# Performance work log

Measured on AMD Instinct MI355X. Metric: run time of the kernel, lower is better.

Reference implementation:

```python
import jax, jax.numpy as jnp
import numpy as np

B, C, H, W = 8, 64, 64, 64
HID = 256  # hidden width of gate_strength_fc


def _init_params(key):
    ks = jax.random.split(key, 12)
    s = 0.05
    p = {}
    p['Wq'] = jax.random.normal(ks[0], (C, C), jnp.float32) * s
    p['bq'] = jnp.zeros((C,), jnp.float32)
    p['Wk'] = jax.random.normal(ks[1], (C, C), jnp.float32) * s
    p['bk'] = jnp.zeros((C,), jnp.float32)
    p['Wv'] = jax.random.normal(ks[2], (C, C), jnp.float32) * s
    p['bv'] = jnp.zeros((C,), jnp.float32)
    p['Wg'] = jax.random.normal(ks[3], (C, C), jnp.float32) * s
    p['bg'] = jnp.zeros((C,), jnp.float32)
    p['W1'] = jax.random.normal(ks[4], (HID, C), jnp.float32) * s
    p['b1'] = jnp.zeros((HID,), jnp.float32)
    p['W2'] = jax.random.normal(ks[5], (1, HID), jnp.float32) * s
    p['b2'] = jnp.zeros((1,), jnp.float32)
    return p


def setup_inputs() -> dict:
    key = jax.random.key(0)
    k0, k1, k2, kp = jax.random.split(key, 4)
    x = jax.random.normal(k0, (B, C, H, W), jnp.float32)
    # torch.rand(...) > 0.8 dropout-style mask, precomputed as 0/1 float for determinism
    mask = (jax.random.uniform(k1, (B, 1, H, W), jnp.float32) > 0.8).astype(jnp.float32)
    use_entropy_gate = jax.random.bernoulli(k2, 0.5, (B,))
    inp = {'x': x, 'mask': mask, 'use_entropy_gate': use_entropy_gate}
    inp.update(_init_params(kp))
    return inp


def _conv1x1(w, b, t):
    # 1x1 conv == per-pixel matmul over channels
    return jnp.einsum('oc,bchw->bohw', w, t) + b[None, :, None, None]


def reference(x, mask, use_entropy_gate, Wq, bq, Wk, bk, Wv, bv, Wg, bg, W1, b1, W2, b2):
    b_, c_, h_, w_ = x.shape
    n = h_ * w_
    masked_x = x * mask
    q = _conv1x1(Wq, bq, masked_x).reshape(b_, c_, n).transpose(0, 2, 1)  # [B,N,C]
    k = _conv1x1(Wk, bk, masked_x).reshape(b_, c_, n)                      # [B,C,N]
    v = _conv1x1(Wv, bv, x).reshape(b_, c_, n)                             # [B,C,N]
    attn = jax.nn.softmax(jnp.einsum('bnc,bcm->bnm', q, k), axis=-1)       # [B,N,N]
    out = jnp.einsum('bcn,bmn->bcm', v, attn).reshape(b_, c_, h_, w_)
    hidden = jax.nn.relu(_conv1x1(W1, b1, x))
    gate_strength = jax.nn.sigmoid(_conv1x1(W2, b2, hidden))               # [B,1,H,W]
    gate = jax.nn.sigmoid(_conv1x1(Wg, bg, x))                             # [B,C,H,W]
    flag = use_entropy_gate[:, None, None, None]
    return jnp.where(flag, out * gate * gate_strength, x)
```

## Files before the change

### kernel.cpp

```cpp
#include <hip/hip_runtime.h>
#include <hip/hip_bf16.h>
#include <math.h>

namespace {
constexpr int kB = 8;
constexpr int kC = 64;
constexpr int kN = 4096;
constexpr int kCap = 1280;
constexpr int kQS = 1312;
constexpr int kSplit = 4;
constexpr long kSeg = (long)kB * kC * kN;
typedef __attribute__((ext_vector_type(8))) short short8;
typedef __attribute__((ext_vector_type(4))) float f32x4;
}

__global__ __launch_bounds__(256) void prep_compact_kernel(
    const float* __restrict__ mask,
    const float* __restrict__ Wq, const float* __restrict__ Wk,
    const float* __restrict__ Wv, const float* __restrict__ Wg,
    const float* __restrict__ W1,
    const float* __restrict__ bq, const float* __restrict__ bk,
    const float* __restrict__ bv, const float* __restrict__ bg,
    const float* __restrict__ b1,
    int* __restrict__ p2i, int* __restrict__ cnt,
    __hip_bfloat16* __restrict__ Wfrag, float* __restrict__ bias_all) {
  const int t = threadIdx.x;
  if (blockIdx.x < kB) {
    const int b = blockIdx.x;
    __shared__ int sc_[256];
    const int base = b * kN + t * 16;
    unsigned flags = 0;
    int c16 = 0;
#pragma unroll
    for (int u = 0; u < 16; ++u) {
      const int a = (mask[base + u] != 0.f) ? 1 : 0;
      flags |= (unsigned)a << u;
      c16 += a;
    }
    sc_[t] = c16;
    __syncthreads();
    for (int off = 1; off < 256; off <<= 1) {
      const int v = (t >= off) ? sc_[t - off] : 0;
      __syncthreads();
      sc_[t] += v;
      __syncthreads();
    }
    int rank = sc_[t] - c16;
#pragma unroll
    for (int u = 0; u < 16; ++u) {
      const int n = t * 16 + u;
      const int a = (flags >> u) & 1;
      int r = -1;
      if (a) {
        if (rank < kCap) r = rank;
        rank += 1;
      }
      p2i[b * kN + n] = r;
    }
    if (t == 255) cnt[b] = sc_[255];
    return;
  }
  const int e = (blockIdx.x - kB) * 256 + t;
  const int mt = e >> 7;
  const int ks = (e >> 6) & 1;
  const int lane = e & 63;
  const int m = mt * 16 + (lane & 15);
  const int k0 = ks * 32 + (lane >> 4) * 8;
  const float* Wsrc;
  int row;
  if (m < 64)       { Wsrc = Wq; row = m; }
  else if (m < 128) { Wsrc = Wk; row = m - 64; }
  else if (m < 192) { Wsrc = Wv; row = m - 128; }
  else if (m < 256) { Wsrc = Wg; row = m - 192; }
  else              { Wsrc = W1; row = m - 256; }
#pragma unroll
  for (int j = 0; j < 8; ++j)
    Wfrag[(long)e * 8 + j] = __float2bfloat16(Wsrc[row * kC + k0 + j]);
  if (e < 512) {
    float bb;
    if (e < 64)       bb = bq[e];
    else if (e < 128) bb = bk[e - 64];
    else if (e < 192) bb = bv[e - 128];
    else if (e < 256) bb = bg[e - 192];
    else              bb = b1[e - 256];
    bias_all[e] = bb;
  }
}

__global__ __launch_bounds__(256) void dense_kernel(
    const float* __restrict__ x, const float* __restrict__ mask,
    const int* __restrict__ flag, const int* __restrict__ p2i,
    const __hip_bfloat16* __restrict__ Wfrag, const float* __restrict__ bias_all,
    const float* __restrict__ W2, const float* __restrict__ b2,
    __hip_bfloat16* __restrict__ G, float* __restrict__ GS,
    __hip_bfloat16* __restrict__ Qa, __hip_bfloat16* __restrict__ Ka,
    __hip_bfloat16* __restrict__ VaT, float* __restrict__ Sq,
    float* __restrict__ xmsP) {
  const int b = blockIdx.y;
  if (!flag[b]) return;
  const int n0 = blockIdx.x * 64;
  const int t = threadIdx.x;

  __shared__ __hip_bfloat16 sX[64][72];
  __shared__ float sB[512];
  __shared__ float sW2[256];
  {
    const int c = t >> 2;
    const int nn = (t & 3) * 16;
    const float* xp = x + (long)b * kC * kN + (long)c * kN + n0 + nn;
#pragma unroll
    for (int u = 0; u < 16; ++u) sX[nn + u][c] = __float2bfloat16(xp[u]);
  }
  sB[t] = bias_all[t];
  sB[t + 256] = bias_all[t + 256];
  sW2[t] = W2[t];
  __syncthreads();

  const int w = t >> 6;
  const int lane = t & 63;
  const int col = lane & 15;
  const int quad = lane >> 4;
  const int nl = w * 16 + col;
  const int n = n0 + nl;

  const short8 bfr0 = *(const short8*)&sX[nl][quad * 8];
  const short8 bfr1 = *(const short8*)&sX[nl][32 + quad * 8];

  const int i_act = p2i[b * kN + n];
  const float b2v = b2[0];

  float gs_acc = 0.f;
  float sq_acc = 0.f;
  for (int mt = 0; mt < 32; ++mt) {
    f32x4 acc = {0.f, 0.f, 0.f, 0.f};
    const short8 a0 = *(const short8*)(Wfrag + (((long)(mt * 2 + 0) * 64 + lane) * 8));
    const short8 a1 = *(const short8*)(Wfrag + (((long)(mt * 2 + 1) * 64 + lane) * 8));
    acc = __builtin_amdgcn_mfma_f32_16x16x32_bf16(a0, bfr0, acc, 0, 0, 0);
    acc = __builtin_amdgcn_mfma_f32_16x16x32_bf16(a1, bfr1, acc, 0, 0, 0);
    const int rbase = mt * 16 + quad * 4;
    if (mt < 4) {
      if (i_act >= 0) {
#pragma unroll
        for (int g = 0; g < 4; ++g) {
          const int r = rbase + g;
          const float qv = acc[g] + sB[r];
          Qa[((long)b * kCap + i_act) * kC + r] = __float2bfloat16(qv);
          sq_acc += qv * sB[64 + r];
        }
      }
    } else if (mt < 8) {
      if (i_act >= 0) {
#pragma unroll
        for (int g = 0; g < 4; ++g) {
          const int r = rbase + g;
          Ka[((long)b * kCap + i_act) * kC + (r - 64)] = __float2bfloat16(acc[g] + sB[r]);
        }
      }
    } else if (mt < 12) {
      if (i_act >= 0) {
#pragma unroll
        for (int g = 0; g < 4; ++g) {
          const int r = rbase + g;
          VaT[((long)b * kC + (r - 128)) * kCap + i_act] =
              __float2bfloat16(acc[g] + sB[r]);
        }
      }
    } else if (mt < 16) {
#pragma unroll
      for (int g = 0; g < 4; ++g) {
        const int r = rbase + g;
        const float gv = 1.f / (1.f + __expf(-(acc[g] + sB[r])));
        G[((long)b * kC + (r - 192)) * kN + n] = __float2bfloat16(gv);
      }
    } else {
#pragma unroll
      for (int g = 0; g < 4; ++g) {
        const int r = rbase + g;
        gs_acc += sW2[r - 256] * fmaxf(acc[g] + sB[r], 0.f);
      }
    }
  }
  gs_acc += __shfl_xor(gs_acc, 16);
  gs_acc += __shfl_xor(gs_acc, 32);
  sq_acc += __shfl_xor(sq_acc, 16);
  sq_acc += __shfl_xor(sq_acc, 32);
  if (quad == 0) {
    GS[(long)b * kN + n] = 1.f / (1.f + __expf(-(gs_acc + b2v)));
    if (i_act >= 0) Sq[(long)b * kCap + i_act] = sq_acc;
  }

  {
    const int c = t >> 2;
    const int g4 = t & 3;
    const float* mp = mask + (long)b * kN + n0 + g4 * 16;
    float s = 0.f;
#pragma unroll
    for (int u = 0; u < 16; ++u)
      if (mp[u] == 0.f) s += __bfloat162float(sX[g4 * 16 + u][c]);
    s += __shfl_xor(s, 1);
    s += __shfl_xor(s, 2);
    if (g4 == 0) xmsP[((long)b * 64 + blockIdx.x) * kC + c] = s;
  }
}

__global__ __launch_bounds__(64) void attn_act_kernel(
    const __hip_bfloat16* __restrict__ Qa, const __hip_bfloat16* __restrict__ Ka,
    const __hip_bfloat16* __restrict__ VaT,
    const int* __restrict__ cnt, const int* __restrict__ flag,
    const float* __restrict__ bq, const float* __restrict__ bk,
    const float* __restrict__ bv, const float* __restrict__ Wv,
    const float* __restrict__ xmsP,
    float* __restrict__ Pm, float* __restrict__ Pl,
    __hip_bfloat16* __restrict__ Po,
    float* __restrict__ Vsum, float* __restrict__ s0M) {
  const int b = blockIdx.z;
  if (!flag[b]) return;
  const int lane = threadIdx.x;

  __shared__ __hip_bfloat16 sP[16][40];
  __shared__ float sxm[kC];

  if (blockIdx.x == kQS / 16) {
    if (blockIdx.y != 0) return;
    float acc = 0.f;
    for (int k = 0; k < 64; ++k) acc += xmsP[((long)b * 64 + k) * kC + lane];
    sxm[lane] = acc;
    __syncthreads();
    float v = 0.f;
#pragma unroll
    for (int o = 0; o < kC; ++o) v += Wv[lane * kC + o] * sxm[o];
    Vsum[b * kC + lane] = v + (float)(kN - cnt[b]) * bv[lane];
    float pp = bq[lane] * bk[lane];
#pragma unroll
    for (int d = 1; d < 64; d <<= 1) pp += __shfl_xor(pp, d);
    if (lane == 0) s0M[0] = pp;
    return;
  }

  const int cc = min(cnt[b], kCap);
  const int ccq = cc + 1;
  const int q0 = blockIdx.x * 16;
  if (q0 >= ccq) return;
  const int s = blockIdx.y;
  const int col = lane & 15;
  const int quad = lane >> 4;
  const int gq = q0 + col;

  const int nT = (cc + 31) >> 5;
  const int tq = (nT + kSplit - 1) / kSplit;
  const int t0 = s * tq;
  const int t1 = min(t0 + tq, nT);
  const long pb = ((long)b * kSplit + s) * kQS + gq;

  if (t0 >= t1) {
    if (gq < ccq) {
      if (quad == 0) { Pm[pb] = -3e38f; Pl[pb] = 0.f; }
#pragma unroll
      for (int ct = 0; ct < 4; ++ct)
#pragma unroll
        for (int g = 0; g < 4; ++g)
          Po[pb * kC + ct * 16 + quad * 4 + g] = __float2bfloat16(0.f);
    }
    return;
  }

  short8 qf0, qf1;
  if (gq == cc) {
#pragma unroll
    for (int j = 0; j < 8; ++j) {
      ((__hip_bfloat16*)&qf0)[j] = __float2bfloat16(bq[quad * 8 + j]);
      ((__hip_bfloat16*)&qf1)[j] = __float2bfloat16(bq[32 + quad * 8 + j]);
    }
  } else {
    const int qrow = (gq < cc) ? gq : (cc - 1);
    const __hip_bfloat16* qr = Qa + ((long)b * kCap + qrow) * kC + quad * 8;
    qf0 = *(const short8*)(qr);
    qf1 = *(const short8*)(qr + 32);
  }

  float Mi = -3e38f, Li = 0.f;
  f32x4 oacc[4];
#pragma unroll
  for (int ct = 0; ct < 4; ++ct) oacc[ct] = (f32x4){0.f, 0.f, 0.f, 0.f};

  for (int kt = t0; kt < t1; ++kt) {
    const int i0 = kt * 32;
    const int kr0 = min(i0 + col, cc - 1);
    const int kr1 = min(i0 + 16 + col, cc - 1);
    const __hip_bfloat16* kp0 = Ka + ((long)b * kCap + kr0) * kC + quad * 8;
    const __hip_bfloat16* kp1 = Ka + ((long)b * kCap + kr1) * kC + quad * 8;
    const short8 kf00 = *(const short8*)(kp0);
    const short8 kf01 = *(const short8*)(kp0 + 32);
    const short8 kf10 = *(const short8*)(kp1);
    const short8 kf11 = *(const short8*)(kp1 + 32);

    f32x4 sa0 = {0.f, 0.f, 0.f, 0.f}, sa1 = {0.f, 0.f, 0.f, 0.f};
    sa0 = __builtin_amdgcn_mfma_f32_16x16x32_bf16(kf00, qf0, sa0, 0, 0, 0);
    sa0 = __builtin_amdgcn_mfma_f32_16x16x32_bf16(kf01, qf1, sa0, 0, 0, 0);
    sa1 = __builtin_amdgcn_mfma_f32_16x16x32_bf16(kf10, qf0, sa1, 0, 0, 0);
    sa1 = __builtin_amdgcn_mfma_f32_16x16x32_bf16(kf11, qf1, sa1, 0, 0, 0);

    float sc[8];
#pragma unroll
    for (int g = 0; g < 4; ++g) {
      sc[g]     = (i0 + quad * 4 + g < cc)      ? sa0[g] : -3e38f;
      sc[4 + g] = (i0 + 16 + quad * 4 + g < cc) ? sa1[g] : -3e38f;
    }
    float lm = sc[0];
#pragma unroll
    for (int u = 1; u < 8; ++u) lm = fmaxf(lm, sc[u]);
    lm = fmaxf(lm, __shfl_xor(lm, 16));
    lm = fmaxf(lm, __shfl_xor(lm, 32));
    const float newM = fmaxf(Mi, lm);
    const float alpha = __expf(Mi - newM);
    float p[8], ps = 0.f;
#pragma unroll
    for (int u = 0; u < 8; ++u) { p[u] = __expf(sc[u] - newM); ps += p[u]; }
    ps += __shfl_xor(ps, 16);
    ps += __shfl_xor(ps, 32);
    Li = Li * alpha + ps;
    Mi = newM;

#pragma unroll
    for (int g = 0; g < 4; ++g) {
      sP[col][quad * 4 + g] = __float2bfloat16(p[g]);
      sP[col][16 + quad * 4 + g] = __float2bfloat16(p[4 + g]);
    }
    __syncthreads();
    const short8 pf = *(const short8*)&sP[col][quad * 8];

#pragma unroll
    for (int ct = 0; ct < 4; ++ct)
#pragma unroll
      for (int g = 0; g < 4; ++g) oacc[ct][g] *= alpha;
#pragma unroll
    for (int ct = 0; ct < 4; ++ct) {
      const short8 vf = *(const short8*)(
          VaT + ((long)b * kC + ct * 16 + col) * kCap + i0 + quad * 8);
      oacc[ct] = __builtin_amdgcn_mfma_f32_16x16x32_bf16(vf, pf, oacc[ct], 0, 0, 0);
    }
    __syncthreads();
  }

  if (gq < ccq) {
    if (quad == 0) { Pm[pb] = Mi; Pl[pb] = Li; }
#pragma unroll
    for (int ct = 0; ct < 4; ++ct)
#pragma unroll
      for (int g = 0; g < 4; ++g)
        Po[pb * kC + ct * 16 + quad * 4 + g] = __float2bfloat16(oacc[ct][g]);
  }
}

__global__ __launch_bounds__(256) void epilogue_kernel(
    const float* __restrict__ x, const int* __restrict__ flag,
    const int* __restrict__ p2i, const int* __restrict__ cnt,
    const float* __restrict__ Pm, const float* __restrict__ Pl,
    const __hip_bfloat16* __restrict__ Po, const float* __restrict__ Sq,
    const float* __restrict__ s0M, const float* __restrict__ Vsum,
    const __hip_bfloat16* __restrict__ G, const float* __restrict__ GS,
    float* __restrict__ out) {
  const int b = blockIdx.z;
  const int cg = blockIdx.y;
  const int n = blockIdx.x * 256 + threadIdx.x;
  const int t = threadIdx.x;
  const long bbase = (long)b * kC * kN + n;
  if (!flag[b]) {
#pragma unroll
    for (int u = 0; u < 16; ++u) {
      const long a = bbase + (long)(cg * 16 + u) * kN;
      out[a] = x[a];
    }
    return;
  }
  const int cTrue = cnt[b];
  const int cc = min(cTrue, kCap);
  const float multF = (float)(kN - cTrue);

  __shared__ float sFac[5];
  __shared__ float sOM16[16];
  __shared__ float sVs[16];
  if (t == 0) {
    const float s0 = s0M[0];
    float mar[kSplit], lar[kSplit];
    float M = s0;
#pragma unroll
    for (int s = 0; s < kSplit; ++s) {
      const long pbs = ((long)b * kSplit + s) * kQS + cc;
      mar[s] = Pm[pbs];
      lar[s] = Pl[pbs];
      M = fmaxf(M, mar[s]);
    }
    const float p0 = __expf(s0 - M);
    float L = multF * p0;
    float wgt[kSplit];
#pragma unroll
    for (int s = 0; s < kSplit; ++s) { wgt[s] = __expf(mar[s] - M); L += lar[s] * wgt[s]; }
    const float invL = 1.f / L;
#pragma unroll
    for (int s = 0; s < kSplit; ++s) sFac[s] = wgt[s] * invL;
    sFac[4] = p0 * invL;
  }
  if (t < 16) sVs[t] = Vsum[b * kC + cg * 16 + t];
  __syncthreads();
  if (t < 16) {
    const int c = cg * 16 + t;
    float o = sFac[4] * sVs[t];
#pragma unroll
    for (int s = 0; s < kSplit; ++s)
      o += sFac[s] * __bfloat162float(Po[(((long)b * kSplit + s) * kQS + cc) * kC + c]);
    sOM16[t] = o;
  }
  __syncthreads();

  const float gsv = GS[(long)b * kN + n];
  const int i = p2i[b * kN + n];
  float fac[kSplit], facP = 0.f;
  if (i >= 0) {
    const float s0 = Sq[(long)b * kCap + i];
    float mar[kSplit], lar[kSplit];
    float M = s0;
#pragma unroll
    for (int s = 0; s < kSplit; ++s) {
      const long pbs = ((long)b * kSplit + s) * kQS + i;
      mar[s] = Pm[pbs];
      lar[s] = Pl[pbs];
      M = fmaxf(M, mar[s]);
    }
    const float p0 = __expf(s0 - M);
    float L = multF * p0;
#pragma unroll
    for (int s = 0; s < kSplit; ++s) { fac[s] = __expf(mar[s] - M); L += lar[s] * fac[s]; }
    const float invL = 1.f / L;
#pragma unroll
    for (int s = 0; s < kSplit; ++s) fac[s] *= invL;
    facP = p0 * invL;
  }
#pragma unroll
  for (int u = 0; u < 16; ++u) {
    const int c = cg * 16 + u;
    float r;
    if (i >= 0) {
      r = facP * sVs[u];
#pragma unroll
      for (int s = 0; s < kSplit; ++s)
        r += fac[s] * __bfloat162float(Po[(((long)b * kSplit + s) * kQS + i) * kC + c]);
    } else {
      r = sOM16[u];
    }
    const long a = bbase + (long)c * kN;
    out[a] = r * __bfloat162float(G[a]) * gsv;
  }
}

extern "C" void kernel_launch(void* const* d_in, const int* in_sizes, int n_in,
                              void* d_out, int out_size, void* d_ws, size_t ws_size,
                              hipStream_t stream) {
  (void)in_sizes; (void)n_in; (void)out_size; (void)ws_size;
  const float* x    = (const float*)d_in[0];
  const float* mask = (const float*)d_in[1];
  const int*   flag = (const int*)d_in[2];
  const float* Wq = (const float*)d_in[3];
  const float* bq = (const float*)d_in[4];
  const float* Wk = (const float*)d_in[5];
  const float* bk = (const float*)d_in[6];
  const float* Wv = (const float*)d_in[7];
  const float* bv = (const float*)d_in[8];
  const float* Wg = (const float*)d_in[9];
  const float* bg = (const float*)d_in[10];
  const float* W1 = (const float*)d_in[11];
  const float* b1 = (const float*)d_in[12];
  const float* W2 = (const float*)d_in[13];
  const float* b2 = (const float*)d_in[14];
  float* out = (float*)d_out;

  char* w = (char*)d_ws;
  float* GS = (float*)w;                       w += (long)kB * kN * 4;
  __hip_bfloat16* G  = (__hip_bfloat16*)w;     w += kSeg * 2;
  __hip_bfloat16* Qa = (__hip_bfloat16*)w;     w += (long)kB * kCap * kC * 2;
  __hip_bfloat16* Ka = (__hip_bfloat16*)w;     w += (long)kB * kCap * kC * 2;
  __hip_bfloat16* VaT= (__hip_bfloat16*)w;     w += (long)kB * kC * kCap * 2;
  __hip_bfloat16* Po = (__hip_bfloat16*)w;     w += (long)kB * kSplit * kQS * kC * 2;
  float* Pm = (float*)w;                       w += (long)kB * kSplit * kQS * 4;
  float* Pl = (float*)w;                       w += (long)kB * kSplit * kQS * 4;
  float* Sq = (float*)w;                       w += (long)kB * kCap * 4;
  float* xmsP = (float*)w;                     w += (long)kB * 64 * kC * 4;
  __hip_bfloat16* Wfrag=(__hip_bfloat16*)w;    w += (long)512 * 64 * 2;
  float* bias_all = (float*)w;                 w += 512 * 4;
  int* p2i = (int*)w;                          w += (long)kB * kN * 4;
  int* cnt = (int*)w;                          w += 64;
  float* Vsum = (float*)w;                     w += kB * kC * 4;
  float* s0M  = (float*)w;                     w += 64;

  prep_compact_kernel<<<kB + 16, 256, 0, stream>>>(
      mask, Wq, Wk, Wv, Wg, W1, bq, bk, bv, bg, b1, p2i, cnt, Wfrag, bias_all);
  dim3 gd(kN / 64, kB);
  dense_kernel<<<gd, 256, 0, stream>>>(x, mask, flag, p2i, Wfrag, bias_all, W2, b2,
                                       G, GS, Qa, Ka, VaT, Sq, xmsP);
  dim3 gat(kQS / 16 + 1, kSplit, kB);
  attn_act_kernel<<<gat, 64, 0, stream>>>(Qa, Ka, VaT, cnt, flag, bq, bk, bv, Wv,
                                          xmsP, Pm, Pl, Po, Vsum, s0M);
  dim3 gep(kN / 256, 4, kB);
  epilogue_kernel<<<gep, 256, 0, stream>>>(x, flag, p2i, cnt, Pm, Pl, Po, Sq,
                                           s0M, Vsum, G, GS, out);
}
```

Baseline: 129.4 us.

## Fuse all stages into one cooperative persistent kernel with grid syncs

Replaces the four separate launches (prep/compact, dense projections, attention, epilogue) with a single cooperative kernel of 512 blocks that moves between phases using grid-wide syncs. Mask compaction is now done per tile with a prefix count plus ballot instead of a separate scan kernel. Weights are converted to bf16 fragments on the fly rather than prepacked. The attention phase uses per-wave shared buffers and no longer needs block barriers. The aim is to remove launch gaps and inter-kernel drain, at the cost of grid sync overhead, redundant prefix counting over the mask, and limited parallelism in the attention phase.

```diff
diff --git a/kernel.cpp b/kernel.cpp
--- a/kernel.cpp
+++ b/kernel.cpp
@@ -1,6 +1,9 @@
 #include <hip/hip_runtime.h>
+#include <hip/hip_cooperative_groups.h>
 #include <hip/hip_bf16.h>
 #include <math.h>
+
+namespace cg = cooperative_groups;
 
 namespace {
 constexpr int kB = 8;
@@ -9,447 +12,405 @@
 constexpr int kCap = 1280;
 constexpr int kQS = 1312;
 constexpr int kSplit = 4;
+constexpr int kQT = kQS / 16;
+constexpr int kAttnW = kQT * kSplit * kB;
+constexpr int kGrid = 512;
 constexpr long kSeg = (long)kB * kC * kN;
 typedef __attribute__((ext_vector_type(8))) short short8;
 typedef __attribute__((ext_vector_type(4))) float f32x4;
 }
 
-__global__ __launch_bounds__(256) void prep_compact_kernel(
-    const float* __restrict__ mask,
-    const float* __restrict__ Wq, const float* __restrict__ Wk,
-    const float* __restrict__ Wv, const float* __restrict__ Wg,
-    const float* __restrict__ W1,
-    const float* __restrict__ bq, const float* __restrict__ bk,
-    const float* __restrict__ bv, const float* __restrict__ bg,
-    const float* __restrict__ b1,
-    int* __restrict__ p2i, int* __restrict__ cnt,
-    __hip_bfloat16* __restrict__ Wfrag, float* __restrict__ bias_all) {
+__global__ __launch_bounds__(256, 2) void fused_kernel(
+    const float* __restrict__ x, const float* __restrict__ mask,
+    const int* __restrict__ flag,
+    const float* __restrict__ Wq, const float* __restrict__ bq,
+    const float* __restrict__ Wk, const float* __restrict__ bk,
+    const float* __restrict__ Wv, const float* __restrict__ bv,
+    const float* __restrict__ Wg, const float* __restrict__ bg,
+    const float* __restrict__ W1, const float* __restrict__ b1,
+    const float* __restrict__ W2, const float* __restrict__ b2,
+    float* __restrict__ out,
+    float* __restrict__ GS, __hip_bfloat16* __restrict__ G,
+    __hip_bfloat16* __restrict__ Qa, __hip_bfloat16* __restrict__ Ka,
+    __hip_bfloat16* __restrict__ VaT,
+    __hip_bfloat16* __restrict__ Po, float* __restrict__ Pm,
+    float* __restrict__ Pl, float* __restrict__ Sq,
+    float* __restrict__ xmsP, int* __restrict__ p2i, int* __restrict__ cnt,
+    float* __restrict__ Vsum, float* __restrict__ s0M) {
   const int t = threadIdx.x;
-  if (blockIdx.x < kB) {
-    const int b = blockIdx.x;
-    __shared__ int sc_[256];
-    const int base = b * kN + t * 16;
-    unsigned flags = 0;
-    int c16 = 0;
-#pragma unroll
-    for (int u = 0; u < 16; ++u) {
-      const int a = (mask[base + u] != 0.f) ? 1 : 0;
-      flags |= (unsigned)a << u;
-      c16 += a;
-    }
-    sc_[t] = c16;
-    __syncthreads();
-    for (int off = 1; off < 256; off <<= 1) {
-      const int v = (t >= off) ? sc_[t - off] : 0;
-      __syncthreads();
-      sc_[t] += v;
-      __syncthreads();
-    }
-    int rank = sc_[t] - c16;
-#pragma unroll
-    for (int u = 0; u < 16; ++u) {
-      const int n = t * 16 + u;
-      const int a = (flags >> u) & 1;
-      int r = -1;
-      if (a) {
-        if (rank < kCap) r = rank;
-        rank += 1;
-      }
-      p2i[b * kN + n] = r;
-    }
-    if (t == 255) cnt[b] = sc_[255];
-    return;
-  }
-  const int e = (blockIdx.x - kB) * 256 + t;
-  const int mt = e >> 7;
-  const int ks = (e >> 6) & 1;
-  const int lane = e & 63;
-  const int m = mt * 16 + (lane & 15);
-  const int k0 = ks * 32 + (lane >> 4) * 8;
-  const float* Wsrc;
-  int row;
-  if (m < 64)       { Wsrc = Wq; row = m; }
-  else if (m < 128) { Wsrc = Wk; row = m - 64; }
-  else if (m < 192) { Wsrc = Wv; row = m - 128; }
-  else if (m < 256) { Wsrc = Wg; row = m - 192; }
-  else              { Wsrc = W1; row = m - 256; }
-#pragma unroll
-  for (int j = 0; j < 8; ++j)
-    Wfrag[(long)e * 8 + j] = __float2bfloat16(Wsrc[row * kC + k0 + j]);
-  if (e < 512) {
-    float bb;
-    if (e < 64)       bb = bq[e];
-    else if (e < 128) bb = bk[e - 64];
-    else if (e < 192) bb = bv[e - 128];
-    else if (e < 256) bb = bg[e - 192];
-    else              bb = b1[e - 256];
-    bias_all[e] = bb;
-  }
-}
-
-__global__ __launch_bounds__(256) void dense_kernel(
-    const float* __restrict__ x, const float* __restrict__ mask,
-    const int* __restrict__ flag, const int* __restrict__ p2i,
-    const __hip_bfloat16* __restrict__ Wfrag, const float* __restrict__ bias_all,
-    const float* __restrict__ W2, const float* __restrict__ b2,
-    __hip_bfloat16* __restrict__ G, float* __restrict__ GS,
-    __hip_bfloat16* __restrict__ Qa, __hip_bfloat16* __restrict__ Ka,
-    __hip_bfloat16* __restrict__ VaT, float* __restrict__ Sq,
-    float* __restrict__ xmsP) {
-  const int b = blockIdx.y;
-  if (!flag[b]) return;
-  const int n0 = blockIdx.x * 64;
-  const int t = threadIdx.x;
+  const int wid = t >> 6;
+  const int lane = t & 63;
 
   __shared__ __hip_bfloat16 sX[64][72];
   __shared__ float sB[512];
   __shared__ float sW2[256];
-  {
-    const int c = t >> 2;
-    const int nn = (t & 3) * 16;
-    const float* xp = x + (long)b * kC * kN + (long)c * kN + n0 + nn;
-#pragma unroll
-    for (int u = 0; u < 16; ++u) sX[nn + u][c] = __float2bfloat16(xp[u]);
-  }
-  sB[t] = bias_all[t];
-  sB[t + 256] = bias_all[t + 256];
-  sW2[t] = W2[t];
-  __syncthreads();
-
-  const int w = t >> 6;
-  const int lane = t & 63;
-  const int col = lane & 15;
-  const int quad = lane >> 4;
-  const int nl = w * 16 + col;
-  const int n = n0 + nl;
-
-  const short8 bfr0 = *(const short8*)&sX[nl][quad * 8];
-  const short8 bfr1 = *(const short8*)&sX[nl][32 + quad * 8];
-
-  const int i_act = p2i[b * kN + n];
-  const float b2v = b2[0];
-
-  float gs_acc = 0.f;
-  float sq_acc = 0.f;
-  for (int mt = 0; mt < 32; ++mt) {
-    f32x4 acc = {0.f, 0.f, 0.f, 0.f};
-    const short8 a0 = *(const short8*)(Wfrag + (((long)(mt * 2 + 0) * 64 + lane) * 8));
-    const short8 a1 = *(const short8*)(Wfrag + (((long)(mt * 2 + 1) * 64 + lane) * 8));
-    acc = __builtin_amdgcn_mfma_f32_16x16x32_bf16(a0, bfr0, acc, 0, 0, 0);
-    acc = __builtin_amdgcn_mfma_f32_16x16x32_bf16(a1, bfr1, acc, 0, 0, 0);
-    const int rbase = mt * 16 + quad * 4;
-    if (mt < 4) {
-      if (i_act >= 0) {
-#pragma unroll
-        for (int g = 0; g < 4; ++g) {
-          const int r = rbase + g;
-          const float qv = acc[g] + sB[r];
-          Qa[((long)b * kCap + i_act) * kC + r] = __float2bfloat16(qv);
-          sq_acc += qv * sB[64 + r];
-        }
-      }
-    } else if (mt < 8) {
-      if (i_act >= 0) {
-#pragma unroll
-        for (int g = 0; g < 4; ++g) {
-          const int r = rbase + g;
-          Ka[((long)b * kCap + i_act) * kC + (r - 64)] = __float2bfloat16(acc[g] + sB[r]);
-        }
-      }
-    } else if (mt < 12) {
-      if (i_act >= 0) {
-#pragma unroll
-        for (int g = 0; g < 4; ++g) {
-          const int r = rbase + g;
-          VaT[((long)b * kC + (r - 128)) * kCap + i_act] =
-              __float2bfloat16(acc[g] + sB[r]);
-        }
-      }
-    } else if (mt < 16) {
-#pragma unroll
-      for (int g = 0; g < 4; ++g) {
-        const int r = rbase + g;
-        const float gv = 1.f / (1.f + __expf(-(acc[g] + sB[r])));
-        G[((long)b * kC + (r - 192)) * kN + n] = __float2bfloat16(gv);
-      }
-    } else {
-#pragma unroll
-      for (int g = 0; g < 4; ++g) {
-        const int r = rbase + g;
-        gs_acc += sW2[r - 256] * fmaxf(acc[g] + sB[r], 0.f);
-      }
-    }
-  }
-  gs_acc += __shfl_xor(gs_acc, 16);
-  gs_acc += __shfl_xor(gs_acc, 32);
-  sq_acc += __shfl_xor(sq_acc, 16);
-  sq_acc += __shfl_xor(sq_acc, 32);
-  if (quad == 0) {
-    GS[(long)b * kN + n] = 1.f / (1.f + __expf(-(gs_acc + b2v)));
-    if (i_act >= 0) Sq[(long)b * kCap + i_act] = sq_acc;
-  }
-
-  {
-    const int c = t >> 2;
-    const int g4 = t & 3;
-    const float* mp = mask + (long)b * kN + n0 + g4 * 16;
-    float s = 0.f;
-#pragma unroll
-    for (int u = 0; u < 16; ++u)
-      if (mp[u] == 0.f) s += __bfloat162float(sX[g4 * 16 + u][c]);
-    s += __shfl_xor(s, 1);
-    s += __shfl_xor(s, 2);
-    if (g4 == 0) xmsP[((long)b * 64 + blockIdx.x) * kC + c] = s;
-  }
-}
-
-__global__ __launch_bounds__(64) void attn_act_kernel(
-    const __hip_bfloat16* __restrict__ Qa, const __hip_bfloat16* __restrict__ Ka,
-    const __hip_bfloat16* __restrict__ VaT,
-    const int* __restrict__ cnt, const int* __restrict__ flag,
-    const float* __restrict__ bq, const float* __restrict__ bk,
-    const float* __restrict__ bv, const float* __restrict__ Wv,
-    const float* __restrict__ xmsP,
-    float* __restrict__ Pm, float* __restrict__ Pl,
-    __hip_bfloat16* __restrict__ Po,
-    float* __restrict__ Vsum, float* __restrict__ s0M) {
-  const int b = blockIdx.z;
-  if (!flag[b]) return;
-  const int lane = threadIdx.x;
-
-  __shared__ __hip_bfloat16 sP[16][40];
-  __shared__ float sxm[kC];
-
-  if (blockIdx.x == kQS / 16) {
-    if (blockIdx.y != 0) return;
-    float acc = 0.f;
-    for (int k = 0; k < 64; ++k) acc += xmsP[((long)b * 64 + k) * kC + lane];
-    sxm[lane] = acc;
-    __syncthreads();
-    float v = 0.f;
-#pragma unroll
-    for (int o = 0; o < kC; ++o) v += Wv[lane * kC + o] * sxm[o];
-    Vsum[b * kC + lane] = v + (float)(kN - cnt[b]) * bv[lane];
-    float pp = bq[lane] * bk[lane];
-#pragma unroll
-    for (int d = 1; d < 64; d <<= 1) pp += __shfl_xor(pp, d);
-    if (lane == 0) s0M[0] = pp;
-    return;
-  }
-
-  const int cc = min(cnt[b], kCap);
-  const int ccq = cc + 1;
-  const int q0 = blockIdx.x * 16;
-  if (q0 >= ccq) return;
-  const int s = blockIdx.y;
-  const int col = lane & 15;
-  const int quad = lane >> 4;
-  const int gq = q0 + col;
-
-  const int nT = (cc + 31) >> 5;
-  const int tq = (nT + kSplit - 1) / kSplit;
-  const int t0 = s * tq;
-  const int t1 = min(t0 + tq, nT);
-  const long pb = ((long)b * kSplit + s) * kQS + gq;
-
-  if (t0 >= t1) {
-    if (gq < ccq) {
-      if (quad == 0) { Pm[pb] = -3e38f; Pl[pb] = 0.f; }
-#pragma unroll
-      for (int ct = 0; ct < 4; ++ct)
-#pragma unroll
-        for (int g = 0; g < 4; ++g)
-          Po[pb * kC + ct * 16 + quad * 4 + g] = __float2bfloat16(0.f);
-    }
-    return;
-  }
-
-  short8 qf0, qf1;
-  if (gq == cc) {
-#pragma unroll
-    for (int j = 0; j < 8; ++j) {
-      ((__hip_bfloat16*)&qf0)[j] = __float2bfloat16(bq[quad * 8 + j]);
-      ((__hip_bfloat16*)&qf1)[j] = __float2bfloat16(bq[32 + quad * 8 + j]);
-    }
-  } else {
-    const int qrow = (gq < cc) ? gq : (cc - 1);
-    const __hip_bfloat16* qr = Qa + ((long)b * kCap + qrow) * kC + quad * 8;
-    qf0 = *(const short8*)(qr);
-    qf1 = *(const short8*)(qr + 32);
-  }
-
-  float Mi = -3e38f, Li = 0.f;
-  f32x4 oacc[4];
-#pragma unroll
-  for (int ct = 0; ct < 4; ++ct) oacc[ct] = (f32x4){0.f, 0.f, 0.f, 0.f};
-
-  for (int kt = t0; kt < t1; ++kt) {
-    const int i0 = kt * 32;
-    const int kr0 = min(i0 + col, cc - 1);
-    const int kr1 = min(i0 + 16 + col, cc - 1);
-    const __hip_bfloat16* kp0 = Ka + ((long)b * kCap + kr0) * kC + quad * 8;
-    const __hip_bfloat16* kp1 = Ka + ((long)b * kCap + kr1) * kC + quad * 8;
-    const short8 kf00 = *(const short8*)(kp0);
-    const short8 kf01 = *(const short8*)(kp0 + 32);
-    const short8 kf10 = *(const short8*)(kp1);
-    const short8 kf11 = *(const short8*)(kp1 + 32);
-
-    f32x4 sa0 = {0.f, 0.f, 0.f, 0.f}, sa1 = {0.f, 0.f, 0.f, 0.f};
-    sa0 = __builtin_amdgcn_mfma_f32_16x16x32_bf16(kf00, qf0, sa0, 0, 0, 0);
-    sa0 = __builtin_amdgcn_mfma_f32_16x16x32_bf16(kf01, qf1, sa0, 0, 0, 0);
-    sa1 = __builtin_amdgcn_mfma_f32_16x16x32_bf16(kf10, qf0, sa1, 0, 0, 0);
-    sa1 = __builtin_amdgcn_mfma_f32_16x16x32_bf16(kf11, qf1, sa1, 0, 0, 0);
-
-    float sc[8];
-#pragma unroll
-    for (int g = 0; g < 4; ++g) {
-      sc[g]     = (i0 + quad * 4 + g < cc)      ? sa0[g] : -3e38f;
-      sc[4 + g] = (i0 + 16 + quad * 4 + g < cc) ? sa1[g] : -3e38f;
-    }
-    float lm = sc[0];
-#pragma unroll
-    for (int u = 1; u < 8; ++u) lm = fmaxf(lm, sc[u]);
-    lm = fmaxf(lm, __shfl_xor(lm, 16));
-    lm = fmaxf(lm, __shfl_xor(lm, 32));
-    const float newM = fmaxf(Mi, lm);
-    const float alpha = __expf(Mi - newM);
-    float p[8], ps = 0.f;
-#pragma unroll
-    for (int u = 0; u < 8; ++u) { p[u] = __expf(sc[u] - newM); ps += p[u]; }
-    ps += __shfl_xor(ps, 16);
-    ps += __shfl_xor(ps, 32);
-    Li = Li * alpha + ps;
-    Mi = newM;
-
-#pragma unroll
-    for (int g = 0; g < 4; ++g) {
-      sP[col][quad * 4 + g] = __float2bfloat16(p[g]);
-      sP[col][16 + quad * 4 + g] = __float2bfloat16(p[4 + g]);
-    }
-    __syncthreads();
-    const short8 pf = *(const short8*)&sP[col][quad * 8];
-
-#pragma unroll
-    for (int ct = 0; ct < 4; ++ct)
-#pragma unroll
-      for (int g = 0; g < 4; ++g) oacc[ct][g] *= alpha;
-#pragma unroll
-    for (int ct = 0; ct < 4; ++ct) {
-      const short8 vf = *(const short8*)(
-          VaT + ((long)b * kC + ct * 16 + col) * kCap + i0 + quad * 8);
-      oacc[ct] = __builtin_amdgcn_mfma_f32_16x16x32_bf16(vf, pf, oacc[ct], 0, 0, 0);
-    }
-    __syncthreads();
-  }
-
-  if (gq < ccq) {
-    if (quad == 0) { Pm[pb] = Mi; Pl[pb] = Li; }
-#pragma unroll
-    for (int ct = 0; ct < 4; ++ct)
-#pragma unroll
-      for (int g = 0; g < 4; ++g)
-        Po[pb * kC + ct * 16 + quad * 4 + g] = __float2bfloat16(oacc[ct][g]);
-  }
-}
-
-__global__ __launch_bounds__(256) void epilogue_kernel(
-    const float* __restrict__ x, const int* __restrict__ flag,
-    const int* __restrict__ p2i, const int* __restrict__ cnt,
-    const float* __restrict__ Pm, const float* __restrict__ Pl,
-    const __hip_bfloat16* __restrict__ Po, const float* __restrict__ Sq,
-    const float* __restrict__ s0M, const float* __restrict__ Vsum,
-    const __hip_bfloat16* __restrict__ G, const float* __restrict__ GS,
-    float* __restrict__ out) {
-  const int b = blockIdx.z;
-  const int cg = blockIdx.y;
-  const int n = blockIdx.x * 256 + threadIdx.x;
-  const int t = threadIdx.x;
-  const long bbase = (long)b * kC * kN + n;
-  if (!flag[b]) {
-#pragma unroll
-    for (int u = 0; u < 16; ++u) {
-      const long a = bbase + (long)(cg * 16 + u) * kN;
-      out[a] = x[a];
-    }
-    return;
-  }
-  const int cTrue = cnt[b];
-  const int cc = min(cTrue, kCap);
-  const float multF = (float)(kN - cTrue);
-
+  __shared__ __hip_bfloat16 sP[4][16][40];
+  __shared__ int sRed[4];
+  __shared__ int sI[64];
   __shared__ float sFac[5];
   __shared__ float sOM16[16];
   __shared__ float sVs[16];
-  if (t == 0) {
-    const float s0 = s0M[0];
-    float mar[kSplit], lar[kSplit];
-    float M = s0;
-#pragma unroll
-    for (int s = 0; s < kSplit; ++s) {
-      const long pbs = ((long)b * kSplit + s) * kQS + cc;
-      mar[s] = Pm[pbs];
-      lar[s] = Pl[pbs];
-      M = fmaxf(M, mar[s]);
-    }
-    const float p0 = __expf(s0 - M);
-    float L = multF * p0;
-    float wgt[kSplit];
-#pragma unroll
-    for (int s = 0; s < kSplit; ++s) { wgt[s] = __expf(mar[s] - M); L += lar[s] * wgt[s]; }
-    const float invL = 1.f / L;
-#pragma unroll
-    for (int s = 0; s < kSplit; ++s) sFac[s] = wgt[s] * invL;
-    sFac[4] = p0 * invL;
+
+  {
+    const int vb = blockIdx.x;
+    const int b = vb >> 6;
+    const int tile = vb & 63;
+    const int n0 = tile * 64;
+    if (flag[b]) {
+      {
+        const int c = t >> 2;
+        const int nn = (t & 3) * 16;
+        const float* xp = x + (long)b * kC * kN + (long)c * kN + n0 + nn;
+#pragma unroll
+        for (int u = 0; u < 16; ++u) sX[nn + u][c] = __float2bfloat16(xp[u]);
+      }
+      if (t < 64) { sB[t] = bq[t]; sB[64 + t] = bk[t]; sB[128 + t] = bv[t]; sB[192 + t] = bg[t]; }
+      sB[256 + t] = b1[t];
+      sW2[t] = W2[t];
+      int loc = 0;
+      for (int n = t; n < n0; n += 256) loc += (mask[b * kN + n] != 0.f) ? 1 : 0;
+#pragma unroll
+      for (int d = 1; d < 64; d <<= 1) loc += __shfl_xor(loc, d);
+      if (lane == 0) sRed[wid] = loc;
+      __syncthreads();
+      const int pbase = sRed[0] + sRed[1] + sRed[2] + sRed[3];
+      if (wid == 0) {
+        const bool a = mask[b * kN + n0 + lane] != 0.f;
+        const unsigned long long bal = __ballot(a);
+        int ia = a ? (pbase + (int)__popcll(bal & ((1ULL << lane) - 1ULL))) : -1;
+        if (ia >= kCap) ia = -1;
+        sI[lane] = ia;
+        p2i[b * kN + n0 + lane] = ia;
+        if (tile == 63 && lane == 0) cnt[b] = pbase + (int)__popcll(bal);
+      }
+      __syncthreads();
+
+      const int col = lane & 15;
+      const int quad = lane >> 4;
+      const int nl = wid * 16 + col;
+      const int n = n0 + nl;
+      const short8 bfr0 = *(const short8*)&sX[nl][quad * 8];
+      const short8 bfr1 = *(const short8*)&sX[nl][32 + quad * 8];
+      const int i_act = sI[nl];
+      const float b2v = b2[0];
+
+      float gs_acc = 0.f, sq_acc = 0.f;
+      for (int mt = 0; mt < 32; ++mt) {
+        const float* Wsrc; int rb0;
+        if (mt < 4)       { Wsrc = Wq; rb0 = mt * 16; }
+        else if (mt < 8)  { Wsrc = Wk; rb0 = (mt - 4) * 16; }
+        else if (mt < 12) { Wsrc = Wv; rb0 = (mt - 8) * 16; }
+        else if (mt < 16) { Wsrc = Wg; rb0 = (mt - 12) * 16; }
+        else              { Wsrc = W1; rb0 = (mt - 16) * 16; }
+        const float* wp = Wsrc + (rb0 + col) * kC + quad * 8;
+        short8 a0, a1;
+#pragma unroll
+        for (int j = 0; j < 8; ++j) {
+          ((__hip_bfloat16*)&a0)[j] = __float2bfloat16(wp[j]);
+          ((__hip_bfloat16*)&a1)[j] = __float2bfloat16(wp[32 + j]);
+        }
+        f32x4 acc = {0.f, 0.f, 0.f, 0.f};
+        acc = __builtin_amdgcn_mfma_f32_16x16x32_bf16(a0, bfr0, acc, 0, 0, 0);
+        acc = __builtin_amdgcn_mfma_f32_16x16x32_bf16(a1, bfr1, acc, 0, 0, 0);
+        const int rbase = mt * 16 + quad * 4;
+        if (mt < 4) {
+          if (i_act >= 0) {
+#pragma unroll
+            for (int g = 0; g < 4; ++g) {
+              const int r = rbase + g;
+              const float qv = acc[g] + sB[r];
+              Qa[((long)b * kCap + i_act) * kC + r] = __float2bfloat16(qv);
+              sq_acc += qv * sB[64 + r];
+            }
+          }
+        } else if (mt < 8) {
+          if (i_act >= 0) {
+#pragma unroll
+            for (int g = 0; g < 4; ++g) {
+              const int r = rbase + g;
+              Ka[((long)b * kCap + i_act) * kC + (r - 64)] = __float2bfloat16(acc[g] + sB[r]);
+            }
+          }
+        } else if (mt < 12) {
+          if (i_act >= 0) {
+#pragma unroll
+            for (int g = 0; g < 4; ++g) {
+              const int r = rbase + g;
+              VaT[((long)b * kC + (r - 128)) * kCap + i_act] =
+                  __float2bfloat16(acc[g] + sB[r]);
+            }
+          }
+        } else if (mt < 16) {
+#pragma unroll
+          for (int g = 0; g < 4; ++g) {
+            const int r = rbase + g;
+            const float gv = 1.f / (1.f + __expf(-(acc[g] + sB[r])));
+            G[((long)b * kC + (r - 192)) * kN + n] = __float2bfloat16(gv);
+          }
+        } else {
+#pragma unroll
+          for (int g = 0; g < 4; ++g) {
+            const int r = rbase + g;
+            gs_acc += sW2[r - 256] * fmaxf(acc[g] + sB[r], 0.f);
+          }
+        }
+      }
+      gs_acc += __shfl_xor(gs_acc, 16);
+      gs_acc += __shfl_xor(gs_acc, 32);
+      sq_acc += __shfl_xor(sq_acc, 16);
+      sq_acc += __shfl_xor(sq_acc, 32);
+      if (quad == 0) {
+        GS[(long)b * kN + n] = 1.f / (1.f + __expf(-(gs_acc + b2v)));
+        if (i_act >= 0) Sq[(long)b * kCap + i_act] = sq_acc;
+      }
+      {
+        const int c = t >> 2;
+        const int g4 = t & 3;
+        const float* mp = mask + (long)b * kN + n0 + g4 * 16;
+        float s = 0.f;
+#pragma unroll
+        for (int u = 0; u < 16; ++u)
+          if (mp[u] == 0.f) s += __bfloat162float(sX[g4 * 16 + u][c]);
+        s += __shfl_xor(s, 1);
+        s += __shfl_xor(s, 2);
+        if (g4 == 0) xmsP[((long)b * 64 + tile) * kC + c] = s;
+      }
+    }
   }
-  if (t < 16) sVs[t] = Vsum[b * kC + cg * 16 + t];
-  __syncthreads();
-  if (t < 16) {
-    const int c = cg * 16 + t;
-    float o = sFac[4] * sVs[t];
-#pragma unroll
-    for (int s = 0; s < kSplit; ++s)
-      o += sFac[s] * __bfloat162float(Po[(((long)b * kSplit + s) * kQS + cc) * kC + c]);
-    sOM16[t] = o;
+  __threadfence();
+  cg::this_grid().sync();
+
+  {
+    const int gw = (blockIdx.x * 256 + t) >> 6;
+    const int nW = (kGrid * 256) >> 6;
+    __hip_bfloat16(*sPw)[40] = sP[wid];
+    for (int vw = gw; vw < kAttnW + kB; vw += nW) {
+      if (vw >= kAttnW) {
+        const int b = vw - kAttnW;
+        if (!flag[b]) continue;
+        float accv = 0.f;
+        for (int k2 = 0; k2 < 64; ++k2) accv += xmsP[((long)b * 64 + k2) * kC + lane];
+        float* sxm = (float*)&sPw[0][0];
+        sxm[lane] = accv;
+        float v = 0.f;
+#pragma unroll
+        for (int o = 0; o < kC; ++o) v += Wv[lane * kC + o] * sxm[o];
+        Vsum[b * kC + lane] = v + (float)(kN - cnt[b]) * bv[lane];
+        float pp = bq[lane] * bk[lane];
+#pragma unroll
+        for (int d = 1; d < 64; d <<= 1) pp += __shfl_xor(pp, d);
+        if (lane == 0) s0M[0] = pp;
+        continue;
+      }
+      const int b = vw / (kQT * kSplit);
+      const int r = vw - b * (kQT * kSplit);
+      const int s = r / kQT;
+      const int qt = r - s * kQT;
+      if (!flag[b]) continue;
+      const int cc = min(cnt[b], kCap);
+      const int ccq = cc + 1;
+      const int q0 = qt * 16;
+      if (q0 >= ccq) continue;
+      const int col = lane & 15;
+      const int quad = lane >> 4;
+      const int gq = q0 + col;
+
+      const int nT = (cc + 31) >> 5;
+      const int tq = (nT + kSplit - 1) / kSplit;
+      const int t0 = s * tq;
+      const int t1 = min(t0 + tq, nT);
+      const long pb = ((long)b * kSplit + s) * kQS + gq;
+
+      if (t0 >= t1) {
+        if (gq < ccq) {
+          if (quad == 0) { Pm[pb] = -3e38f; Pl[pb] = 0.f; }
+#pragma unroll
+          for (int ct = 0; ct < 4; ++ct)
+#pragma unroll
+            for (int g = 0; g < 4; ++g)
+              Po[pb * kC + ct * 16 + quad * 4 + g] = __float2bfloat16(0.f);
+        }
+        continue;
+      }
+
+      short8 qf0, qf1;
+      if (gq == cc) {
+#pragma unroll
+        for (int j = 0; j < 8; ++j) {
+          ((__hip_bfloat16*)&qf0)[j] = __float2bfloat16(bq[quad * 8 + j]);
+          ((__hip_bfloat16*)&qf1)[j] = __float2bfloat16(bq[32 + quad * 8 + j]);
+        }
+      } else {
+        const int qrow = (gq < cc) ? gq : (cc - 1);
+        const __hip_bfloat16* qr = Qa + ((long)b * kCap + qrow) * kC + quad * 8;
+        qf0 = *(const short8*)(qr);
+        qf1 = *(const short8*)(qr + 32);
+      }
+
+      float Mi = -3e38f, Li = 0.f;
+      f32x4 oacc[4];
+#pragma unroll
+      for (int ct = 0; ct < 4; ++ct) oacc[ct] = (f32x4){0.f, 0.f, 0.f, 0.f};
+
+      for (int kt = t0; kt < t1; ++kt) {
+        const int i0 = kt * 32;
+        const int kr0 = min(i0 + col, cc - 1);
+        const int kr1 = min(i0 + 16 + col, cc - 1);
+        const __hip_bfloat16* kp0 = Ka + ((long)b * kCap + kr0) * kC + quad * 8;
+        const __hip_bfloat16* kp1 = Ka + ((long)b * kCap + kr1) * kC + quad * 8;
+        const short8 kf00 = *(const short8*)(kp0);
+        const short8 kf01 = *(const short8*)(kp0 + 32);
+        const short8 kf10 = *(const short8*)(kp1);
+        const short8 kf11 = *(const short8*)(kp1 + 32);
+
+        f32x4 sa0 = {0.f, 0.f, 0.f, 0.f}, sa1 = {0.f, 0.f, 0.f, 0.f};
+        sa0 = __builtin_amdgcn_mfma_f32_16x16x32_bf16(kf00, qf0, sa0, 0, 0, 0);
+        sa0 = __builtin_amdgcn_mfma_f32_16x16x32_bf16(kf01, qf1, sa0, 0, 0, 0);
+        sa1 = __builtin_amdgcn_mfma_f32_16x16x32_bf16(kf10, qf0, sa1, 0, 0, 0);
+        sa1 = __builtin_amdgcn_mfma_f32_16x16x32_bf16(kf11, qf1, sa1, 0, 0, 0);
+
+        float sc[8];
+#pragma unroll
+        for (int g = 0; g < 4; ++g) {
+          sc[g]     = (i0 + quad * 4 + g < cc)      ? sa0[g] : -3e38f;
+          sc[4 + g] = (i0 + 16 + quad * 4 + g < cc) ? sa1[g] : -3e38f;
+        }
+        float lm = sc[0];
+#pragma unroll
+        for (int u = 1; u < 8; ++u) lm = fmaxf(lm, sc[u]);
+        lm = fmaxf(lm, __shfl_xor(lm, 16));
+        lm = fmaxf(lm, __shfl_xor(lm, 32));
+        const float newM = fmaxf(Mi, lm);
+        const float alpha = __expf(Mi - newM);
+        float p[8], ps = 0.f;
+#pragma unroll
+        for (int u = 0; u < 8; ++u) { p[u] = __expf(sc[u] - newM); ps += p[u]; }
+        ps += __shfl_xor(ps, 16);
+        ps += __shfl_xor(ps, 32);
+        Li = Li * alpha + ps;
+        Mi = newM;
+
+#pragma unroll
+        for (int g = 0; g < 4; ++g) {
+          sPw[col][quad * 4 + g] = __float2bfloat16(p[g]);
+          sPw[col][16 + quad * 4 + g] = __float2bfloat16(p[4 + g]);
+        }
+        const short8 pf = *(const short8*)&sPw[col][quad * 8];
+
+#pragma unroll
+        for (int ct = 0; ct < 4; ++ct)
+#pragma unroll
+          for (int g = 0; g < 4; ++g) oacc[ct][g] *= alpha;
+#pragma unroll
+        for (int ct = 0; ct < 4; ++ct) {
+          const short8 vf = *(const short8*)(
+              VaT + ((long)b * kC + ct * 16 + col) * kCap + i0 + quad * 8);
+          oacc[ct] = __builtin_amdgcn_mfma_f32_16x16x32_bf16(vf, pf, oacc[ct], 0, 0, 0);
+        }
+      }
+
+      if (gq < ccq) {
+        if (quad == 0) { Pm[pb] = Mi; Pl[pb] = Li; }
+#pragma unroll
+        for (int ct = 0; ct < 4; ++ct)
+#pragma unroll
+          for (int g = 0; g < 4; ++g)
+            Po[pb * kC + ct * 16 + quad * 4 + g] = __float2bfloat16(oacc[ct][g]);
+      }
+    }
   }
-  __syncthreads();
-
-  const float gsv = GS[(long)b * kN + n];
-  const int i = p2i[b * kN + n];
-  float fac[kSplit], facP = 0.f;
-  if (i >= 0) {
-    const float s0 = Sq[(long)b * kCap + i];
-    float mar[kSplit], lar[kSplit];
-    float M = s0;
-#pragma unroll
-    for (int s = 0; s < kSplit; ++s) {
-      const long pbs = ((long)b * kSplit + s) * kQS + i;
-      mar[s] = Pm[pbs];
-      lar[s] = Pl[pbs];
-      M = fmaxf(M, mar[s]);
-    }
-    const float p0 = __expf(s0 - M);
-    float L = multF * p0;
-#pragma unroll
-    for (int s = 0; s < kSplit; ++s) { fac[s] = __expf(mar[s] - M); L += lar[s] * fac[s]; }
-    const float invL = 1.f / L;
-#pragma unroll
-    for (int s = 0; s < kSplit; ++s) fac[s] *= invL;
-    facP = p0 * invL;
-  }
-#pragma unroll
-  for (int u = 0; u < 16; ++u) {
-    const int c = cg * 16 + u;
-    float r;
+  __threadfence();
+  cg::this_grid().sync();
+
+  {
+    const int vb = blockIdx.x;
+    const int b = vb >> 6;
+    const int cgi = (vb >> 4) & 3;
+    const int n = (vb & 15) * 256 + t;
+    const long bbase = (long)b * kC * kN + n;
+    if (!flag[b]) {
+#pragma unroll
+      for (int u = 0; u < 16; ++u) {
+        const long a = bbase + (long)(cgi * 16 + u) * kN;
+        out[a] = x[a];
+      }
+      return;
+    }
+    const int cTrue = cnt[b];
+    const int cc = min(cTrue, kCap);
+    const float multF = (float)(kN - cTrue);
+
+    if (t == 0) {
+      const float s0 = s0M[0];
+      float mar[kSplit], lar[kSplit];
+      float M = s0;
+#pragma unroll
+      for (int s = 0; s < kSplit; ++s) {
+        const long pbs = ((long)b * kSplit + s) * kQS + cc;
+        mar[s] = Pm[pbs];
+        lar[s] = Pl[pbs];
+        M = fmaxf(M, mar[s]);
+      }
+      const float p0 = __expf(s0 - M);
+      float L = multF * p0;
+      float wgt[kSplit];
+#pragma unroll
+      for (int s = 0; s < kSplit; ++s) { wgt[s] = __expf(mar[s] - M); L += lar[s] * wgt[s]; }
+      const float invL = 1.f / L;
+#pragma unroll
+      for (int s = 0; s < kSplit; ++s) sFac[s] = wgt[s] * invL;
+      sFac[4] = p0 * invL;
+    }
+    if (t < 16) sVs[t] = Vsum[b * kC + cgi * 16 + t];
+    __syncthreads();
+    if (t < 16) {
+      const int c = cgi * 16 + t;
+      float o = sFac[4] * sVs[t];
+#pragma unroll
+      for (int s = 0; s < kSplit; ++s)
+        o += sFac[s] * __bfloat162float(Po[(((long)b * kSplit + s) * kQS + cc) * kC + c]);
+      sOM16[t] = o;
+    }
+    __syncthreads();
+
+    const float gsv = GS[(long)b * kN + n];
+    const int i = p2i[b * kN + n];
+    float fac[kSplit], facP = 0.f;
     if (i >= 0) {
-      r = facP * sVs[u];
-#pragma unroll
-      for (int s = 0; s < kSplit; ++s)
-        r += fac[s] * __bfloat162float(Po[(((long)b * kSplit + s) * kQS + i) * kC + c]);
-    } else {
-      r = sOM16[u];
-    }
-    const long a = bbase + (long)c * kN;
-    out[a] = r * __bfloat162float(G[a]) * gsv;
+      const float s0 = Sq[(long)b * kCap + i];
+      float mar[kSplit], lar[kSplit];
+      float M = s0;
+#pragma unroll
+      for (int s = 0; s < kSplit; ++s) {
+        const long pbs = ((long)b * kSplit + s) * kQS + i;
+        mar[s] = Pm[pbs];
+        lar[s] = Pl[pbs];
+        M = fmaxf(M, mar[s]);
+      }
+      const float p0 = __expf(s0 - M);
+      float L = multF * p0;
+#pragma unroll
+      for (int s = 0; s < kSplit; ++s) { fac[s] = __expf(mar[s] - M); L += lar[s] * fac[s]; }
+      const float invL = 1.f / L;
+#pragma unroll
+      for (int s = 0; s < kSplit; ++s) fac[s] *= invL;
+      facP = p0 * invL;
+    }
+#pragma unroll
+    for (int u = 0; u < 16; ++u) {
+      const int c = cgi * 16 + u;
+      float rr;
+      if (i >= 0) {
+        rr = facP * sVs[u];
+#pragma unroll
+        for (int s = 0; s < kSplit; ++s)
+          rr += fac[s] * __bfloat162float(Po[(((long)b * kSplit + s) * kQS + i) * kC + c]);
+      } else {
+        rr = sOM16[u];
+      }
+      const long a = bbase + (long)c * kN;
+      out[a] = rr * __bfloat162float(G[a]) * gsv;
+    }
   }
 }
 
@@ -485,22 +446,20 @@
   float* Pl = (float*)w;                       w += (long)kB * kSplit * kQS * 4;
   float* Sq = (float*)w;                       w += (long)kB * kCap * 4;
   float* xmsP = (float*)w;                     w += (long)kB * 64 * kC * 4;
-  __hip_bfloat16* Wfrag=(__hip_bfloat16*)w;    w += (long)512 * 64 * 2;
-  float* bias_all = (float*)w;                 w += 512 * 4;
   int* p2i = (int*)w;                          w += (long)kB * kN * 4;
   int* cnt = (int*)w;                          w += 64;
   float* Vsum = (float*)w;                     w += kB * kC * 4;
   float* s0M  = (float*)w;                     w += 64;
 
-  prep_compact_kernel<<<kB + 16, 256, 0, stream>>>(
-      mask, Wq, Wk, Wv, Wg, W1, bq, bk, bv, bg, b1, p2i, cnt, Wfrag, bias_all);
-  dim3 gd(kN / 64, kB);
-  dense_kernel<<<gd, 256, 0, stream>>>(x, mask, flag, p2i, Wfrag, bias_all, W2, b2,
-                                       G, GS, Qa, Ka, VaT, Sq, xmsP);
-  dim3 gat(kQS / 16 + 1, kSplit, kB);
-  attn_act_kernel<<<gat, 64, 0, stream>>>(Qa, Ka, VaT, cnt, flag, bq, bk, bv, Wv,
-                                          xmsP, Pm, Pl, Po, Vsum, s0M);
-  dim3 gep(kN / 256, 4, kB);
-  epilogue_kernel<<<gep, 256, 0, stream>>>(x, flag, p2i, cnt, Pm, Pl, Po, Sq,
-                                           s0M, Vsum, G, GS, out);
+  void* kargs[] = {
+      (void*)&x,  (void*)&mask, (void*)&flag,
+      (void*)&Wq, (void*)&bq,  (void*)&Wk, (void*)&bk,
+      (void*)&Wv, (void*)&bv,  (void*)&Wg, (void*)&bg,
+      (void*)&W1, (void*)&b1,  (void*)&W2, (void*)&b2,
+      (void*)&out,
+      (void*)&GS, (void*)&G,   (void*)&Qa, (void*)&Ka, (void*)&VaT,
+      (void*)&Po, (void*)&Pm,  (void*)&Pl, (void*)&Sq,
+      (void*)&xmsP, (void*)&p2i, (void*)&cnt, (void*)&Vsum, (void*)&s0M};
+  hipLaunchCooperativeKernel((const void*)fused_kernel, dim3(kGrid), dim3(256),
+                             kargs, 0, stream);
 }
```

Measured after the change: 368.3 us. +184.7%, slower.
